# Performance work log

Hardware: AMD Instinct MI355X
Metric: run time of the kernel (lower is better)

The kernel has to match this reference:

```python
import jax, jax.numpy as jnp
import numpy as np

NUM_EMBEDDINGS = 512
EMBEDDING_DIM = 128
COMMITMENT_COST = 0.25
DECAY = 0.99
EPSILON = 1e-5


def setup_inputs() -> dict:
    key = jax.random.key(0)
    k1, k2 = jax.random.split(key)
    inputs = jax.random.normal(k1, (2, EMBEDDING_DIM, 32, 32, 32), dtype=jnp.float32)
    embedding_w = jax.random.normal(k2, (NUM_EMBEDDINGS, EMBEDDING_DIM), dtype=jnp.float32)
    ema_cluster_size = jnp.zeros((NUM_EMBEDDINGS,), dtype=jnp.float32)
    ema_w = embedding_w  # buffer initialized as a clone of the codebook
    return {"inputs": inputs, "embedding_w": embedding_w,
            "ema_cluster_size": ema_cluster_size, "ema_w": ema_w}


def reference(inputs, embedding_w, ema_cluster_size, ema_w):
    B, C, D, H, W = inputs.shape
    K = embedding_w.shape[0]

    # flatten: channel-last then [N, C]
    flat_input = jnp.transpose(inputs, (0, 2, 3, 4, 1)).reshape(-1, C)  # [N, C]
    N = flat_input.shape[0]

    # squared-euclidean distances to the codebook: [N, K]
    distances = ((flat_input ** 2).sum(axis=1, keepdims=True)
                 + (embedding_w ** 2).sum(axis=1)[None, :]
                 - 2.0 * flat_input @ embedding_w.T)

    encoding_indices = jnp.argmax(-distances, axis=1)  # [N] int32

    # entropy regularizer over soft assignments (temperature 1.0)
    probs = jax.nn.softmax(-distances, axis=1)
    entropy_loss = 0.01 * (-jnp.sum(probs * jnp.log(probs + 1e-8)) / N)

    # embed: gather codebook rows, reshape to channel-first volume
    quantized_raw = embedding_w[encoding_indices].reshape(B, D, H, W, C)
    quantized_raw = jnp.transpose(quantized_raw, (0, 4, 1, 2, 3))  # [B, C, D, H, W]

    # commitment loss (codebook is EMA-updated, not grad-updated)
    commit_loss = COMMITMENT_COST * jnp.mean(
        (jax.lax.stop_gradient(quantized_raw) - inputs) ** 2)
    loss = commit_loss + entropy_loss

    # straight-through estimator output
    quantized = inputs + jax.lax.stop_gradient(quantized_raw - inputs)

    # EMA codebook update (scatter-add over argmin clusters)
    encodings_sum = jnp.zeros((K,), flat_input.dtype).at[encoding_indices].add(1.0)
    dw = jnp.zeros((K, C), flat_input.dtype).at[encoding_indices].add(flat_input)
    new_cluster_size = DECAY * ema_cluster_size + (1.0 - DECAY) * encodings_sum
    n_total = new_cluster_size.sum()
    smoothed = (new_cluster_size + EPSILON) / (n_total + K * EPSILON) * n_total
    new_ema_w = DECAY * ema_w + (1.0 - DECAY) * dw
    new_embedding_w = new_ema_w / smoothed[:, None]

    encoding_indices_vol = encoding_indices.reshape(B, D, H, W)
    return (quantized, loss, encoding_indices_vol,
            new_cluster_size, new_ema_w, new_embedding_w)
```

## Files before the change

kernel.cpp:

```cpp
#include <hip/hip_runtime.h>

#define LOSS_OFF  8388608
#define IDX_OFF   8388609
#define NCS_OFF   8454145
#define EMAW_OFF  8454657
#define EMB_OFF   8520193

typedef __attribute__((ext_vector_type(8))) short short8;
typedef __attribute__((ext_vector_type(4))) float f32x4;

__device__ __forceinline__ unsigned short bf16r(float x) {
  unsigned u = __float_as_uint(x);
  u += 0x7fff + ((u >> 16) & 1);
  return (unsigned short)(u >> 16);
}
__device__ __forceinline__ float bf16tof(unsigned short h) {
  return __uint_as_float(((unsigned)h) << 16);
}

__global__ __attribute__((amdgpu_flat_work_group_size(256, 256),
                          amdgpu_waves_per_eu(2, 4)))
void dist_kernel(const float* __restrict__ inputs, const float* __restrict__ emb,
                 float* __restrict__ out, float* __restrict__ idxws,
                 float* __restrict__ sums)
{
  __shared__ __align__(16) short esm[2][2][32 * 136];
  __shared__ float eeS[2][32];
  __shared__ float xxs[128];
  __shared__ int   ibkL[128];
  __shared__ float red[8];
  float* xs = (float*)&esm[0][0][0];

  const int t = threadIdx.x, lane = t & 63, wave = t >> 6;
  const int n0 = blockIdx.x * 128;
  const int b = n0 >> 15, s0 = n0 & 32767;
  const int col = lane & 15, quad = lane >> 4;
  const int kk = t >> 3, c0 = (t & 7) * 16;

  short8 ahi[2][4], alo[2][4];
  for (int r4 = 0; r4 < 4; ++r4) {
    __syncthreads();
    {
      const int rr = t & 31, cc = (t >> 5) * 16;
      const float* src = inputs + (size_t)b * 128 * 32768 + s0 + r4 * 32 + rr;
      #pragma unroll
      for (int i = 0; i < 16; ++i)
        xs[rr * 132 + cc + i] = src[(size_t)(cc + i) * 32768];
    }
    __syncthreads();
    if (wave == r4) {
      #pragma unroll
      for (int rg = 0; rg < 2; ++rg) {
        float xacc = 0.f;
        const float* xr = &xs[(rg * 16 + col) * 132 + quad * 8];
        #pragma unroll
        for (int q = 0; q < 4; ++q) {
          float v[8];
          *(float4*)&v[0] = *(const float4*)(xr + q * 32);
          *(float4*)&v[4] = *(const float4*)(xr + q * 32 + 4);
          short8 h8, l8;
          #pragma unroll
          for (int j = 0; j < 8; ++j) {
            unsigned short hh = bf16r(v[j]);
            h8[j] = (short)hh;
            l8[j] = (short)bf16r(v[j] - bf16tof(hh));
            xacc += v[j] * v[j];
          }
          ahi[rg][q] = h8; alo[rg][q] = l8;
        }
        xacc += __shfl_xor(xacc, 16);
        xacc += __shfl_xor(xacc, 32);
        if (lane < 16) xxs[wave * 32 + rg * 16 + lane] = xacc;
      }
    }
  }
  __syncthreads();

  float mS[8], sS[8], tS[8]; int kS[8];
  #pragma unroll
  for (int i = 0; i < 8; ++i) { mS[i] = 1e30f; sS[i] = 0.f; tS[i] = 0.f; kS[i] = 0; }

  float4 pf0, pf1, pf2, pf3;
  {
    const float* src = emb + (size_t)kk * 128 + c0;
    pf0 = ((const float4*)src)[0]; pf1 = ((const float4*)src)[1];
    pf2 = ((const float4*)src)[2]; pf3 = ((const float4*)src)[3];
    float v[16];
    *(float4*)&v[0] = pf0; *(float4*)&v[4] = pf1;
    *(float4*)&v[8] = pf2; *(float4*)&v[12] = pf3;
    short8 h0, h1, l0, l1; float sq = 0.f;
    #pragma unroll
    for (int j = 0; j < 8; ++j) {
      unsigned short hh = bf16r(v[j]);
      h0[j] = (short)hh; l0[j] = (short)bf16r(v[j] - bf16tof(hh));
      sq += v[j] * v[j];
      unsigned short hh2 = bf16r(v[8 + j]);
      h1[j] = (short)hh2; l1[j] = (short)bf16r(v[8 + j] - bf16tof(hh2));
      sq += v[8 + j] * v[8 + j];
    }
    *(short8*)&esm[0][0][kk * 136 + c0] = h0;
    *(short8*)&esm[0][0][kk * 136 + c0 + 8] = h1;
    *(short8*)&esm[0][1][kk * 136 + c0] = l0;
    *(short8*)&esm[0][1][kk * 136 + c0 + 8] = l1;
    sq += __shfl_xor(sq, 1); sq += __shfl_xor(sq, 2); sq += __shfl_xor(sq, 4);
    if ((t & 7) == 0) eeS[0][kk] = sq;
  }

  for (int st = 0; st < 16; ++st) {
    const int pb = st & 1;
    if (st < 15) {
      const float* src = emb + (size_t)((st + 1) * 32 + kk) * 128 + c0;
      pf0 = ((const float4*)src)[0]; pf1 = ((const float4*)src)[1];
      pf2 = ((const float4*)src)[2]; pf3 = ((const float4*)src)[3];
    }
    __syncthreads();
    #pragma unroll
    for (int kt = 0; kt < 2; ++kt) {
      f32x4 ac0 = {0.f, 0.f, 0.f, 0.f}, ac1 = {0.f, 0.f, 0.f, 0.f};
      const int boff = (kt * 16 + col) * 136 + quad * 8;
      #pragma unroll
      for (int q = 0; q < 4; ++q) {
        short8 bh = *(const short8*)&esm[pb][0][boff + q * 32];
        short8 bl = *(const short8*)&esm[pb][1][boff + q * 32];
        ac0 = __builtin_amdgcn_mfma_f32_16x16x32_bf16(alo[0][q], bh, ac0, 0, 0, 0);
        ac1 = __builtin_amdgcn_mfma_f32_16x16x32_bf16(alo[1][q], bh, ac1, 0, 0, 0);
        ac0 = __builtin_amdgcn_mfma_f32_16x16x32_bf16(ahi[0][q], bl, ac0, 0, 0, 0);
        ac1 = __builtin_amdgcn_mfma_f32_16x16x32_bf16(ahi[1][q], bl, ac1, 0, 0, 0);
        ac0 = __builtin_amdgcn_mfma_f32_16x16x32_bf16(ahi[0][q], bh, ac0, 0, 0, 0);
        ac1 = __builtin_amdgcn_mfma_f32_16x16x32_bf16(ahi[1][q], bh, ac1, 0, 0, 0);
      }
      const int code = st * 32 + kt * 16 + col;
      const float eec = eeS[pb][kt * 16 + col];
      #pragma unroll
      for (int si = 0; si < 8; ++si) {
        float a = (si < 4) ? ac0[si & 3] : ac1[si & 3];
        float d = eec - 2.f * a;
        float mo = mS[si];
        float mn = fminf(mo, d);
        float E  = __expf(mn - fmaxf(mo, d));
        bool nw  = d < mo;
        float f  = nw ? E : 1.f;
        float e2 = nw ? 1.f : E;
        tS[si] = (tS[si] + (mn - mo) * sS[si]) * f + (mn - d) * e2;
        sS[si] = sS[si] * f + e2;
        kS[si] = nw ? code : kS[si];
        mS[si] = mn;
      }
    }
    if (st < 15) {
      const int nb = pb ^ 1;
      float v[16];
      *(float4*)&v[0] = pf0; *(float4*)&v[4] = pf1;
      *(float4*)&v[8] = pf2; *(float4*)&v[12] = pf3;
      short8 h0, h1, l0, l1; float sq = 0.f;
      #pragma unroll
      for (int j = 0; j < 8; ++j) {
        unsigned short hh = bf16r(v[j]);
        h0[j] = (short)hh; l0[j] = (short)bf16r(v[j] - bf16tof(hh));
        sq += v[j] * v[j];
        unsigned short hh2 = bf16r(v[8 + j]);
        h1[j] = (short)hh2; l1[j] = (short)bf16r(v[8 + j] - bf16tof(hh2));
        sq += v[8 + j] * v[8 + j];
      }
      *(short8*)&esm[nb][0][kk * 136 + c0] = h0;
      *(short8*)&esm[nb][0][kk * 136 + c0 + 8] = h1;
      *(short8*)&esm[nb][1][kk * 136 + c0] = l0;
      *(short8*)&esm[nb][1][kk * 136 + c0 + 8] = l1;
      sq += __shfl_xor(sq, 1); sq += __shfl_xor(sq, 2); sq += __shfl_xor(sq, 4);
      if ((t & 7) == 0) eeS[nb][kk] = sq;
    }
  }

  #pragma unroll
  for (int off = 1; off <= 8; off <<= 1) {
    #pragma unroll
    for (int si = 0; si < 8; ++si) {
      float m2 = __shfl_xor(mS[si], off);
      float S2 = __shfl_xor(sS[si], off);
      float T2 = __shfl_xor(tS[si], off);
      int   k2 = __shfl_xor(kS[si], off);
      float mo = mS[si];
      float mn = fminf(mo, m2);
      float f1 = __expf(mn - mo);
      float f2 = __expf(mn - m2);
      tS[si] = (tS[si] + (mn - mo) * sS[si]) * f1 + (T2 + (mn - m2) * S2) * f2;
      sS[si] = sS[si] * f1 + S2 * f2;
      if (m2 < mo || (m2 == mo && k2 < kS[si])) kS[si] = k2;
      mS[si] = mn;
    }
  }

  float cacc = 0.f, eacc = 0.f;
  #pragma unroll
  for (int si = 0; si < 8; ++si) {
    int rg = si >> 2, reg = si & 3;
    int row = wave * 32 + rg * 16 + quad * 4 + reg;
    if (col == 0) {
      float xx = xxs[row];
      int rn = n0 + row;
      float fk = (float)kS[si];
      out[IDX_OFF + rn] = fk;
      idxws[rn] = fk;
      ibkL[row] = kS[si];
      cacc += xx + mS[si];
      eacc += tS[si] / sS[si] - __logf(sS[si]);
    }
  }
  cacc += __shfl_xor(cacc, 16); cacc += __shfl_xor(cacc, 32);
  eacc += __shfl_xor(eacc, 16); eacc += __shfl_xor(eacc, 32);
  if (lane == 0) { red[wave] = cacc; red[4 + wave] = eacc; }
  __syncthreads();
  if (t == 0) {
    unsafeAtomicAdd(&sums[0], red[0] + red[1] + red[2] + red[3]);
    unsafeAtomicAdd(&sums[1], red[4] + red[5] + red[6] + red[7]);
  }

  for (int r4 = 0; r4 < 4; ++r4) {
    __syncthreads();
    {
      const int rr = t & 31, cc = (t >> 5) * 16;
      const int kq = ibkL[r4 * 32 + rr];
      const float* src = emb + (size_t)kq * 128 + cc;
      float4 v0 = *(const float4*)(src);
      float4 v1 = *(const float4*)(src + 4);
      float4 v2 = *(const float4*)(src + 8);
      float4 v3 = *(const float4*)(src + 12);
      float* dst = &xs[rr * 132 + cc];
      *(float4*)dst = v0; *(float4*)(dst + 4) = v1;
      *(float4*)(dst + 8) = v2; *(float4*)(dst + 12) = v3;
    }
    __syncthreads();
    {
      const int l7 = t & 7;
      #pragma unroll
      for (int pp = 0; pp < 4; ++pp) {
        int c = (t >> 3) + 32 * pp;
        float4 v;
        v.x = xs[(4 * l7 + 0) * 132 + c];
        v.y = xs[(4 * l7 + 1) * 132 + c];
        v.z = xs[(4 * l7 + 2) * 132 + c];
        v.w = xs[(4 * l7 + 3) * 132 + c];
        *(float4*)(out + ((size_t)b * 128 + c) * 32768 + s0 + r4 * 32 + 4 * l7) = v;
      }
    }
  }
}

__global__ __launch_bounds__(256) void scatter_kernel(
    const float* __restrict__ inputs, const float* __restrict__ idxws,
    float* __restrict__ partial, float* __restrict__ cpart, int S)
{
  __shared__ float acc[512 * 9];
  __shared__ float cnts[512];
  const int t = threadIdx.x;
  const int s = blockIdx.x >> 4, ccB = blockIdx.x & 15;
  const int R = 65536 / S;
  for (int m = t; m < 512 * 9; m += 256) acc[m] = 0.f;
  if (ccB == 0) for (int m = t; m < 512; m += 256) cnts[m] = 0.f;
  __syncthreads();
  const int l = t & 63, cg = t >> 6;
  for (int it = 0; it < R / 256; ++it) {
    int n = s * R + it * 256;
    int bb = n >> 15;
    int sp = (n & 32767) + 4 * l;
    float4 i4 = *(const float4*)(idxws + n + 4 * l);
    int k0 = (int)i4.x, k1 = (int)i4.y, k2 = (int)i4.z, k3 = (int)i4.w;
    #pragma unroll
    for (int ci = 0; ci < 2; ++ci) {
      int c = cg * 2 + ci;
      float4 x4 = *(const float4*)(inputs + ((size_t)bb * 128 + ccB * 8 + c) * 32768 + sp);
      atomicAdd(&acc[k0 * 9 + c], x4.x);
      atomicAdd(&acc[k1 * 9 + c], x4.y);
      atomicAdd(&acc[k2 * 9 + c], x4.z);
      atomicAdd(&acc[k3 * 9 + c], x4.w);
    }
    if (ccB == 0 && cg == 0) {
      atomicAdd(&cnts[k0], 1.f); atomicAdd(&cnts[k1], 1.f);
      atomicAdd(&cnts[k2], 1.f); atomicAdd(&cnts[k3], 1.f);
    }
  }
  __syncthreads();
  for (int m = t; m < 512 * 8; m += 256) {
    int k = m >> 3, c = m & 7;
    partial[(size_t)s * 65536 + k * 128 + ccB * 8 + c] = acc[k * 9 + c];
  }
  if (ccB == 0) for (int m = t; m < 512; m += 256) cpart[s * 512 + m] = cnts[m];
}

__global__ __launch_bounds__(256) void fin_kernel(const float* __restrict__ ecs,
    const float* __restrict__ emaw, const float* __restrict__ partial,
    const float* __restrict__ cpart, const float* __restrict__ sums,
    float* __restrict__ out, int S)
{
  __shared__ float cn[512];
  __shared__ float rsum[256];
  const int t = threadIdx.x;
  float local = 0.f;
  for (int k = t; k < 512; k += 256) {
    float c = 0.f;
    for (int s = 0; s < S; ++s) c += cpart[s * 512 + k];
    float v = 0.99f * ecs[k] + 0.01f * c;
    cn[k] = v; local += v;
  }
  rsum[t] = local;
  __syncthreads();
  for (int o = 128; o; o >>= 1) {
    if (t < o) rsum[t] += rsum[t + o];
    __syncthreads();
  }
  const float ntot = rsum[0];
  if (blockIdx.x == 0) {
    for (int k = t; k < 512; k += 256) out[NCS_OFF + k] = cn[k];
    if (t == 0)
      out[LOSS_OFF] = 0.25f * sums[0] / 8388608.f - 0.01f * sums[1] / 65536.f;
  }
  const int i = blockIdx.x * 256 + t;
  float dwv = 0.f;
  for (int s = 0; s < S; ++s) dwv += partial[(size_t)s * 65536 + i];
  float val = 0.99f * emaw[i] + 0.01f * dwv;
  const int k = i >> 7;
  float sm = (cn[k] + 1e-5f) / (ntot + 0.00512f) * ntot;
  out[EMAW_OFF + i] = val;
  out[EMB_OFF + i] = val / sm;
}

extern "C" void kernel_launch(void* const* d_in, const int* in_sizes, int n_in,
                              void* d_out, int out_size, void* d_ws, size_t ws_size,
                              hipStream_t stream) {
  const float* inputs = (const float*)d_in[0];
  const float* emb    = (const float*)d_in[1];
  const float* ecs    = (const float*)d_in[2];
  const float* emaw   = (const float*)d_in[3];
  float* out = (float*)d_out;
  float* wsf = (float*)d_ws;
  (void)in_sizes; (void)n_in; (void)out_size;

  size_t wsfl = ws_size / 4;
  int S = 16;
  while (S > 1 && (size_t)S * 66048 + 65552 > wsfl) S >>= 1;

  float* partial = wsf;
  float* cpart   = partial + (size_t)S * 65536;
  float* idxws   = cpart + (size_t)S * 512;
  float* sums    = idxws + 65536;

  hipMemsetAsync(sums, 0, 16 * sizeof(float), stream);
  dist_kernel   <<<512,    256, 0, stream>>>(inputs, emb, out, idxws, sums);
  scatter_kernel<<<16 * S, 256, 0, stream>>>(inputs, idxws, partial, cpart, S);
  fin_kernel    <<<256,    256, 0, stream>>>(ecs, emaw, partial, cpart, sums, out, S);
}
```

Before: 211.6 us.

## Precompute bf16 codebook split, halve dist tile, move gather to separate kernel

Adds a prep kernel that converts the codebook to hi/lo bf16 halves and precomputes norms once, so each dist block no longer re-converts the full codebook. The dist tile shrinks from 128 to 64 rows per block, giving 1024 blocks, and the distances are computed in log2 space using the hardware exp2/log intrinsics. The quantized-output gather moves out of the dist kernel into a separate gather kernel. The scatter split is fixed at 32, and the partial sums are staged in the output buffer before it is overwritten. This trades extra kernel launches and more codebook reloads per output row for higher occupancy and less per-block work.

```diff
diff --git a/kernel.cpp b/kernel.cpp
--- a/kernel.cpp
+++ b/kernel.cpp
@@ -9,6 +9,11 @@
 typedef __attribute__((ext_vector_type(8))) short short8;
 typedef __attribute__((ext_vector_type(4))) float f32x4;
 
+#define LOG2E 1.4426950408889634f
+#define N2L2E -2.8853900817779268f
+#define LN2   0.6931471805599453f
+#define NSPLIT 32
+
 __device__ __forceinline__ unsigned short bf16r(float x) {
   unsigned u = __float_as_uint(x);
   u += 0x7fff + ((u >> 16) & 1);
@@ -18,27 +23,53 @@
   return __uint_as_float(((unsigned)h) << 16);
 }
 
+__global__ __launch_bounds__(256) void prep_kernel(const float* __restrict__ emb,
+    unsigned short* __restrict__ ehig, unsigned short* __restrict__ elog,
+    float* __restrict__ eeg)
+{
+  __shared__ float r1[256];
+  const int t = threadIdx.x;
+  const int k = blockIdx.x * 2 + (t >> 7);
+  const int c = t & 127;
+  float x = emb[k * 128 + c];
+  unsigned short hh = bf16r(x);
+  ehig[k * 128 + c] = hh;
+  elog[k * 128 + c] = bf16r(x - bf16tof(hh));
+  r1[t] = x * x;
+  __syncthreads();
+  #pragma unroll
+  for (int off = 64; off; off >>= 1) {
+    if ((t & 127) < off) r1[t] += r1[t + off];
+    __syncthreads();
+  }
+  if ((t & 127) == 0) eeg[k] = LOG2E * r1[t];
+}
+
 __global__ __attribute__((amdgpu_flat_work_group_size(256, 256),
                           amdgpu_waves_per_eu(2, 4)))
-void dist_kernel(const float* __restrict__ inputs, const float* __restrict__ emb,
+void dist_kernel(const float* __restrict__ inputs,
+                 const unsigned short* __restrict__ ehig,
+                 const unsigned short* __restrict__ elog,
+                 const float* __restrict__ eeg,
                  float* __restrict__ out, float* __restrict__ idxws,
                  float* __restrict__ sums)
 {
   __shared__ __align__(16) short esm[2][2][32 * 136];
-  __shared__ float eeS[2][32];
-  __shared__ float xxs[128];
-  __shared__ int   ibkL[128];
+  __shared__ float eeL[512];
+  __shared__ float xxs[64];
   __shared__ float red[8];
   float* xs = (float*)&esm[0][0][0];
 
   const int t = threadIdx.x, lane = t & 63, wave = t >> 6;
-  const int n0 = blockIdx.x * 128;
+  const int n0 = blockIdx.x * 64;
   const int b = n0 >> 15, s0 = n0 & 32767;
   const int col = lane & 15, quad = lane >> 4;
-  const int kk = t >> 3, c0 = (t & 7) * 16;
-
-  short8 ahi[2][4], alo[2][4];
-  for (int r4 = 0; r4 < 4; ++r4) {
+  const int kk = t >> 3, c0s = (t & 7) * 16;
+
+  eeL[t] = eeg[t]; eeL[256 + t] = eeg[256 + t];
+
+  short8 ahi[4], alo[4];
+  for (int r4 = 0; r4 < 2; ++r4) {
     __syncthreads();
     {
       const int rr = t & 31, cc = (t >> 5) * 16;
@@ -48,96 +79,75 @@
         xs[rr * 132 + cc + i] = src[(size_t)(cc + i) * 32768];
     }
     __syncthreads();
-    if (wave == r4) {
+    if ((wave >> 1) == r4) {
+      float xacc = 0.f;
+      const float* xr = &xs[((wave & 1) * 16 + col) * 132 + quad * 8];
       #pragma unroll
-      for (int rg = 0; rg < 2; ++rg) {
-        float xacc = 0.f;
-        const float* xr = &xs[(rg * 16 + col) * 132 + quad * 8];
+      for (int q = 0; q < 4; ++q) {
+        float v[8];
+        *(float4*)&v[0] = *(const float4*)(xr + q * 32);
+        *(float4*)&v[4] = *(const float4*)(xr + q * 32 + 4);
+        short8 h8, l8;
         #pragma unroll
-        for (int q = 0; q < 4; ++q) {
-          float v[8];
-          *(float4*)&v[0] = *(const float4*)(xr + q * 32);
-          *(float4*)&v[4] = *(const float4*)(xr + q * 32 + 4);
-          short8 h8, l8;
-          #pragma unroll
-          for (int j = 0; j < 8; ++j) {
-            unsigned short hh = bf16r(v[j]);
-            h8[j] = (short)hh;
-            l8[j] = (short)bf16r(v[j] - bf16tof(hh));
-            xacc += v[j] * v[j];
-          }
-          ahi[rg][q] = h8; alo[rg][q] = l8;
+        for (int j = 0; j < 8; ++j) {
+          unsigned short hh = bf16r(v[j]);
+          h8[j] = (short)hh;
+          l8[j] = (short)bf16r(v[j] - bf16tof(hh));
+          xacc += v[j] * v[j];
         }
-        xacc += __shfl_xor(xacc, 16);
-        xacc += __shfl_xor(xacc, 32);
-        if (lane < 16) xxs[wave * 32 + rg * 16 + lane] = xacc;
+        ahi[q] = h8; alo[q] = l8;
       }
-    }
-  }
-  __syncthreads();
-
-  float mS[8], sS[8], tS[8]; int kS[8];
+      xacc += __shfl_xor(xacc, 16);
+      xacc += __shfl_xor(xacc, 32);
+      if (quad == 0) xxs[wave * 16 + col] = xacc;
+    }
+  }
+  __syncthreads();
+
+  uint4 ph0, ph1, pl0, pl1;
+  {
+    const size_t go = (size_t)kk * 128 + c0s;
+    ph0 = ((const uint4*)(ehig + go))[0]; ph1 = ((const uint4*)(ehig + go))[1];
+    pl0 = ((const uint4*)(elog + go))[0]; pl1 = ((const uint4*)(elog + go))[1];
+  }
+  *(uint4*)&esm[0][0][kk * 136 + c0s] = ph0;
+  *(uint4*)&esm[0][0][kk * 136 + c0s + 8] = ph1;
+  *(uint4*)&esm[0][1][kk * 136 + c0s] = pl0;
+  *(uint4*)&esm[0][1][kk * 136 + c0s + 8] = pl1;
+  {
+    const size_t go = (size_t)(32 + kk) * 128 + c0s;
+    ph0 = ((const uint4*)(ehig + go))[0]; ph1 = ((const uint4*)(ehig + go))[1];
+    pl0 = ((const uint4*)(elog + go))[0]; pl1 = ((const uint4*)(elog + go))[1];
+  }
+
+  float mS[4], sS[4], tS[4]; int kS[4];
   #pragma unroll
-  for (int i = 0; i < 8; ++i) { mS[i] = 1e30f; sS[i] = 0.f; tS[i] = 0.f; kS[i] = 0; }
-
-  float4 pf0, pf1, pf2, pf3;
-  {
-    const float* src = emb + (size_t)kk * 128 + c0;
-    pf0 = ((const float4*)src)[0]; pf1 = ((const float4*)src)[1];
-    pf2 = ((const float4*)src)[2]; pf3 = ((const float4*)src)[3];
-    float v[16];
-    *(float4*)&v[0] = pf0; *(float4*)&v[4] = pf1;
-    *(float4*)&v[8] = pf2; *(float4*)&v[12] = pf3;
-    short8 h0, h1, l0, l1; float sq = 0.f;
-    #pragma unroll
-    for (int j = 0; j < 8; ++j) {
-      unsigned short hh = bf16r(v[j]);
-      h0[j] = (short)hh; l0[j] = (short)bf16r(v[j] - bf16tof(hh));
-      sq += v[j] * v[j];
-      unsigned short hh2 = bf16r(v[8 + j]);
-      h1[j] = (short)hh2; l1[j] = (short)bf16r(v[8 + j] - bf16tof(hh2));
-      sq += v[8 + j] * v[8 + j];
-    }
-    *(short8*)&esm[0][0][kk * 136 + c0] = h0;
-    *(short8*)&esm[0][0][kk * 136 + c0 + 8] = h1;
-    *(short8*)&esm[0][1][kk * 136 + c0] = l0;
-    *(short8*)&esm[0][1][kk * 136 + c0 + 8] = l1;
-    sq += __shfl_xor(sq, 1); sq += __shfl_xor(sq, 2); sq += __shfl_xor(sq, 4);
-    if ((t & 7) == 0) eeS[0][kk] = sq;
-  }
+  for (int i = 0; i < 4; ++i) { mS[i] = 1e30f; sS[i] = 0.f; tS[i] = 0.f; kS[i] = 0; }
 
   for (int st = 0; st < 16; ++st) {
     const int pb = st & 1;
-    if (st < 15) {
-      const float* src = emb + (size_t)((st + 1) * 32 + kk) * 128 + c0;
-      pf0 = ((const float4*)src)[0]; pf1 = ((const float4*)src)[1];
-      pf2 = ((const float4*)src)[2]; pf3 = ((const float4*)src)[3];
-    }
     __syncthreads();
     #pragma unroll
     for (int kt = 0; kt < 2; ++kt) {
-      f32x4 ac0 = {0.f, 0.f, 0.f, 0.f}, ac1 = {0.f, 0.f, 0.f, 0.f};
+      f32x4 ac = {0.f, 0.f, 0.f, 0.f};
       const int boff = (kt * 16 + col) * 136 + quad * 8;
       #pragma unroll
       for (int q = 0; q < 4; ++q) {
         short8 bh = *(const short8*)&esm[pb][0][boff + q * 32];
         short8 bl = *(const short8*)&esm[pb][1][boff + q * 32];
-        ac0 = __builtin_amdgcn_mfma_f32_16x16x32_bf16(alo[0][q], bh, ac0, 0, 0, 0);
-        ac1 = __builtin_amdgcn_mfma_f32_16x16x32_bf16(alo[1][q], bh, ac1, 0, 0, 0);
-        ac0 = __builtin_amdgcn_mfma_f32_16x16x32_bf16(ahi[0][q], bl, ac0, 0, 0, 0);
-        ac1 = __builtin_amdgcn_mfma_f32_16x16x32_bf16(ahi[1][q], bl, ac1, 0, 0, 0);
-        ac0 = __builtin_amdgcn_mfma_f32_16x16x32_bf16(ahi[0][q], bh, ac0, 0, 0, 0);
-        ac1 = __builtin_amdgcn_mfma_f32_16x16x32_bf16(ahi[1][q], bh, ac1, 0, 0, 0);
+        ac = __builtin_amdgcn_mfma_f32_16x16x32_bf16(alo[q], bh, ac, 0, 0, 0);
+        ac = __builtin_amdgcn_mfma_f32_16x16x32_bf16(ahi[q], bl, ac, 0, 0, 0);
+        ac = __builtin_amdgcn_mfma_f32_16x16x32_bf16(ahi[q], bh, ac, 0, 0, 0);
       }
       const int code = st * 32 + kt * 16 + col;
-      const float eec = eeS[pb][kt * 16 + col];
+      const float eec2 = eeL[code];
       #pragma unroll
-      for (int si = 0; si < 8; ++si) {
-        float a = (si < 4) ? ac0[si & 3] : ac1[si & 3];
-        float d = eec - 2.f * a;
+      for (int si = 0; si < 4; ++si) {
+        float d  = fmaf(ac[si], N2L2E, eec2);
         float mo = mS[si];
         float mn = fminf(mo, d);
-        float E  = __expf(mn - fmaxf(mo, d));
+        float mx = fmaxf(mo, d);
+        float E  = __builtin_amdgcn_exp2f(mn - mx);
         bool nw  = d < mo;
         float f  = nw ? E : 1.f;
         float e2 = nw ? 1.f : E;
@@ -149,40 +159,30 @@
     }
     if (st < 15) {
       const int nb = pb ^ 1;
-      float v[16];
-      *(float4*)&v[0] = pf0; *(float4*)&v[4] = pf1;
-      *(float4*)&v[8] = pf2; *(float4*)&v[12] = pf3;
-      short8 h0, h1, l0, l1; float sq = 0.f;
-      #pragma unroll
-      for (int j = 0; j < 8; ++j) {
-        unsigned short hh = bf16r(v[j]);
-        h0[j] = (short)hh; l0[j] = (short)bf16r(v[j] - bf16tof(hh));
-        sq += v[j] * v[j];
-        unsigned short hh2 = bf16r(v[8 + j]);
-        h1[j] = (short)hh2; l1[j] = (short)bf16r(v[8 + j] - bf16tof(hh2));
-        sq += v[8 + j] * v[8 + j];
+      *(uint4*)&esm[nb][0][kk * 136 + c0s] = ph0;
+      *(uint4*)&esm[nb][0][kk * 136 + c0s + 8] = ph1;
+      *(uint4*)&esm[nb][1][kk * 136 + c0s] = pl0;
+      *(uint4*)&esm[nb][1][kk * 136 + c0s + 8] = pl1;
+      if (st < 14) {
+        const size_t go = (size_t)((st + 2) * 32 + kk) * 128 + c0s;
+        ph0 = ((const uint4*)(ehig + go))[0]; ph1 = ((const uint4*)(ehig + go))[1];
+        pl0 = ((const uint4*)(elog + go))[0]; pl1 = ((const uint4*)(elog + go))[1];
       }
-      *(short8*)&esm[nb][0][kk * 136 + c0] = h0;
-      *(short8*)&esm[nb][0][kk * 136 + c0 + 8] = h1;
-      *(short8*)&esm[nb][1][kk * 136 + c0] = l0;
-      *(short8*)&esm[nb][1][kk * 136 + c0 + 8] = l1;
-      sq += __shfl_xor(sq, 1); sq += __shfl_xor(sq, 2); sq += __shfl_xor(sq, 4);
-      if ((t & 7) == 0) eeS[nb][kk] = sq;
     }
   }
 
   #pragma unroll
   for (int off = 1; off <= 8; off <<= 1) {
     #pragma unroll
-    for (int si = 0; si < 8; ++si) {
+    for (int si = 0; si < 4; ++si) {
       float m2 = __shfl_xor(mS[si], off);
       float S2 = __shfl_xor(sS[si], off);
       float T2 = __shfl_xor(tS[si], off);
       int   k2 = __shfl_xor(kS[si], off);
       float mo = mS[si];
       float mn = fminf(mo, m2);
-      float f1 = __expf(mn - mo);
-      float f2 = __expf(mn - m2);
+      float f1 = __builtin_amdgcn_exp2f(mn - mo);
+      float f2 = __builtin_amdgcn_exp2f(mn - m2);
       tS[si] = (tS[si] + (mn - mo) * sS[si]) * f1 + (T2 + (mn - m2) * S2) * f2;
       sS[si] = sS[si] * f1 + S2 * f2;
       if (m2 < mo || (m2 == mo && k2 < kS[si])) kS[si] = k2;
@@ -191,19 +191,16 @@
   }
 
   float cacc = 0.f, eacc = 0.f;
-  #pragma unroll
-  for (int si = 0; si < 8; ++si) {
-    int rg = si >> 2, reg = si & 3;
-    int row = wave * 32 + rg * 16 + quad * 4 + reg;
-    if (col == 0) {
-      float xx = xxs[row];
+  if (col == 0) {
+    #pragma unroll
+    for (int si = 0; si < 4; ++si) {
+      int row = wave * 16 + quad * 4 + si;
       int rn = n0 + row;
       float fk = (float)kS[si];
       out[IDX_OFF + rn] = fk;
       idxws[rn] = fk;
-      ibkL[row] = kS[si];
-      cacc += xx + mS[si];
-      eacc += tS[si] / sS[si] - __logf(sS[si]);
+      cacc += xxs[row] + mS[si] * LN2;
+      eacc += LN2 * (tS[si] / sS[si] - __builtin_amdgcn_logf(sS[si]));
     }
   }
   cacc += __shfl_xor(cacc, 16); cacc += __shfl_xor(cacc, 32);
@@ -214,47 +211,17 @@
     unsafeAtomicAdd(&sums[0], red[0] + red[1] + red[2] + red[3]);
     unsafeAtomicAdd(&sums[1], red[4] + red[5] + red[6] + red[7]);
   }
-
-  for (int r4 = 0; r4 < 4; ++r4) {
-    __syncthreads();
-    {
-      const int rr = t & 31, cc = (t >> 5) * 16;
-      const int kq = ibkL[r4 * 32 + rr];
-      const float* src = emb + (size_t)kq * 128 + cc;
-      float4 v0 = *(const float4*)(src);
-      float4 v1 = *(const float4*)(src + 4);
-      float4 v2 = *(const float4*)(src + 8);
-      float4 v3 = *(const float4*)(src + 12);
-      float* dst = &xs[rr * 132 + cc];
-      *(float4*)dst = v0; *(float4*)(dst + 4) = v1;
-      *(float4*)(dst + 8) = v2; *(float4*)(dst + 12) = v3;
-    }
-    __syncthreads();
-    {
-      const int l7 = t & 7;
-      #pragma unroll
-      for (int pp = 0; pp < 4; ++pp) {
-        int c = (t >> 3) + 32 * pp;
-        float4 v;
-        v.x = xs[(4 * l7 + 0) * 132 + c];
-        v.y = xs[(4 * l7 + 1) * 132 + c];
-        v.z = xs[(4 * l7 + 2) * 132 + c];
-        v.w = xs[(4 * l7 + 3) * 132 + c];
-        *(float4*)(out + ((size_t)b * 128 + c) * 32768 + s0 + r4 * 32 + 4 * l7) = v;
-      }
-    }
-  }
 }
 
 __global__ __launch_bounds__(256) void scatter_kernel(
     const float* __restrict__ inputs, const float* __restrict__ idxws,
-    float* __restrict__ partial, float* __restrict__ cpart, int S)
+    float* partial, float* __restrict__ cpart)
 {
   __shared__ float acc[512 * 9];
   __shared__ float cnts[512];
   const int t = threadIdx.x;
   const int s = blockIdx.x >> 4, ccB = blockIdx.x & 15;
-  const int R = 65536 / S;
+  const int R = 65536 / NSPLIT;
   for (int m = t; m < 512 * 9; m += 256) acc[m] = 0.f;
   if (ccB == 0) for (int m = t; m < 512; m += 256) cnts[m] = 0.f;
   __syncthreads();
@@ -288,9 +255,9 @@
 }
 
 __global__ __launch_bounds__(256) void fin_kernel(const float* __restrict__ ecs,
-    const float* __restrict__ emaw, const float* __restrict__ partial,
+    const float* __restrict__ emaw, const float* partial,
     const float* __restrict__ cpart, const float* __restrict__ sums,
-    float* __restrict__ out, int S)
+    float* out)
 {
   __shared__ float cn[512];
   __shared__ float rsum[256];
@@ -298,7 +265,7 @@
   float local = 0.f;
   for (int k = t; k < 512; k += 256) {
     float c = 0.f;
-    for (int s = 0; s < S; ++s) c += cpart[s * 512 + k];
+    for (int s = 0; s < NSPLIT; ++s) c += cpart[s * 512 + k];
     float v = 0.99f * ecs[k] + 0.01f * c;
     cn[k] = v; local += v;
   }
@@ -316,12 +283,46 @@
   }
   const int i = blockIdx.x * 256 + t;
   float dwv = 0.f;
-  for (int s = 0; s < S; ++s) dwv += partial[(size_t)s * 65536 + i];
+  for (int s = 0; s < NSPLIT; ++s) dwv += partial[(size_t)s * 65536 + i];
   float val = 0.99f * emaw[i] + 0.01f * dwv;
   const int k = i >> 7;
   float sm = (cn[k] + 1e-5f) / (ntot + 0.00512f) * ntot;
   out[EMAW_OFF + i] = val;
   out[EMB_OFF + i] = val / sm;
+}
+
+__global__ __launch_bounds__(256) void gather_kernel(const float* __restrict__ emb,
+    const float* __restrict__ idxws, float* __restrict__ out)
+{
+  __shared__ float eq[128 * 64];
+  const int t  = threadIdx.x;
+  const int n0 = blockIdx.x * 64;
+  const int b  = n0 >> 15;
+  const int s0 = n0 & 32767;
+  {
+    const int r  = t >> 2;
+    const int qq = t & 3;
+    const int kidx = (int)idxws[n0 + r];
+    const float* src = emb + (size_t)kidx * 128;
+    #pragma unroll
+    for (int i = 0; i < 8; ++i) {
+      int g = qq + 4 * i;
+      float4 v = *(const float4*)(src + g * 4);
+      float* dst = &eq[(g * 4) * 64 + r];
+      dst[0] = v.x; dst[64] = v.y; dst[128] = v.z; dst[192] = v.w;
+    }
+  }
+  __syncthreads();
+  {
+    const int sl = (t & 15) * 4;
+    const int cb = t >> 4;
+    #pragma unroll
+    for (int j = 0; j < 8; ++j) {
+      int c = cb + 16 * j;
+      float4 v = *(const float4*)&eq[c * 64 + sl];
+      *(float4*)(out + ((size_t)b * 128 + c) * 32768 + s0 + sl) = v;
+    }
+  }
 }
 
 extern "C" void kernel_launch(void* const* d_in, const int* in_sizes, int n_in,
@@ -333,19 +334,19 @@
   const float* emaw   = (const float*)d_in[3];
   float* out = (float*)d_out;
   float* wsf = (float*)d_ws;
-  (void)in_sizes; (void)n_in; (void)out_size;
-
-  size_t wsfl = ws_size / 4;
-  int S = 16;
-  while (S > 1 && (size_t)S * 66048 + 65552 > wsfl) S >>= 1;
-
-  float* partial = wsf;
-  float* cpart   = partial + (size_t)S * 65536;
-  float* idxws   = cpart + (size_t)S * 512;
-  float* sums    = idxws + 65536;
+  (void)in_sizes; (void)n_in; (void)out_size; (void)ws_size;
+
+  float* idxws = wsf;
+  float* sums  = wsf + 65536;
+  float* eeg   = wsf + 65552;
+  unsigned short* ehig = (unsigned short*)(wsf + 66064);
+  unsigned short* elog = ehig + 65536;
+  float* cpart = (float*)(elog + 65536);
 
   hipMemsetAsync(sums, 0, 16 * sizeof(float), stream);
-  dist_kernel   <<<512,    256, 0, stream>>>(inputs, emb, out, idxws, sums);
-  scatter_kernel<<<16 * S, 256, 0, stream>>>(inputs, idxws, partial, cpart, S);
-  fin_kernel    <<<256,    256, 0, stream>>>(ecs, emaw, partial, cpart, sums, out, S);
-}
+  prep_kernel   <<<256,        256, 0, stream>>>(emb, ehig, elog, eeg);
+  dist_kernel   <<<1024,       256, 0, stream>>>(inputs, ehig, elog, eeg, out, idxws, sums);
+  scatter_kernel<<<16 * NSPLIT,256, 0, stream>>>(inputs, idxws, out, cpart);
+  fin_kernel    <<<256,        256, 0, stream>>>(ecs, emaw, out, cpart, sums, out);
+  gather_kernel <<<1024,       256, 0, stream>>>(emb, idxws, out);
+}
```

Result: faster. 199.6 us (-5.7%).
